# Kernel tuning notes

Hardware: AMD Instinct MI355X
Metric: run time of the kernel (lower is better)

## Reference

```python
import jax, jax.numpy as jnp
import numpy as np

NUM_HEADS = 4
NUM_POINTS = 8


def deform_attn_3d(q, value, ref, Hf, Wf, Wv, bv, Wo, bo, Wa, ba):
    # q: (BS,N,C)  value: (BS,Hf*Wf,C)  ref: (BS,N,D,2) normalized (x,y) in [0,1]
    BS, N, C = q.shape
    H, P = NUM_HEADS, NUM_POINTS
    D = ref.shape[2]
    c = C // H
    # value projection, split heads: (BS,H,M,c)
    v = (value @ Wv + bv).reshape(BS, Hf * Wf, H, c).transpose(0, 2, 1, 3)
    # sampling offsets and attention weights from the query
    off = (q @ Wo + bo).reshape(BS, N, H, P, 2)
    attn = jax.nn.softmax((q @ Wa + ba).reshape(BS, N, H, P), axis=-1)
    # normalize offsets by (W,H); distribute P points over D z-anchors (P//D per anchor)
    norm = jnp.array([Wf, Hf], dtype=q.dtype)
    off = off.reshape(BS, N, H, P // D, D, 2) / norm
    loc = (ref[:, :, None, None, :, :] + off).reshape(BS, N, H, P, 2)
    # grid_sample(align_corners=False, padding=zeros): pixel = loc*size - 0.5
    x = loc[..., 0] * Wf - 0.5
    y = loc[..., 1] * Hf - 0.5
    x0f = jnp.floor(x)
    y0f = jnp.floor(y)
    lx = x - x0f
    ly = y - y0f
    x0 = x0f.astype(jnp.int32)
    y0 = y0f.astype(jnp.int32)

    def tohead(a):  # (BS,N,H,P) -> (BS,H,N*P)
        return a.transpose(0, 2, 1, 3).reshape(BS, H, N * P)

    def gather(yy, xx):
        valid = ((xx >= 0) & (xx < Wf) & (yy >= 0) & (yy < Hf)).astype(q.dtype)
        idx = jnp.clip(yy, 0, Hf - 1) * Wf + jnp.clip(xx, 0, Wf - 1)
        g = jnp.take_along_axis(v, tohead(idx)[..., None], axis=2)  # (BS,H,N*P,c)
        return g * tohead(valid)[..., None]

    out = (gather(y0, x0) * tohead((1 - lx) * (1 - ly))[..., None]
           + gather(y0, x0 + 1) * tohead(lx * (1 - ly))[..., None]
           + gather(y0 + 1, x0) * tohead((1 - lx) * ly)[..., None]
           + gather(y0 + 1, x0 + 1) * tohead(lx * ly)[..., None])
    out = (out * tohead(attn)[..., None]).reshape(BS, H, N, P, c).sum(3)  # (BS,H,N,c)
    return out.transpose(0, 2, 1, 3).reshape(BS, N, C)


def spatial_cross_attention(query, query_pos, value, reference_points_cam, bev_mask,
                            Hf, Wf, Wv, bv, Wo, bo, Wa, ba, Wout, bout):
    # query/query_pos: (B,N,C); value: (S,M,B,C); ref: (S,B,N,D,2); bev_mask: (S,B,N,D)
    B, N, C = query.shape
    S, M = value.shape[0], value.shape[1]
    D = reference_points_cam.shape[3]
    q = query + query_pos
    # broadcast queries over cameras (mask-equivalent of the torch rebatch/compaction):
    # deformable attention is per-query independent, so computing all queries per cam
    # and masking invalid ones is the same math as rebatch+scatter.
    q_all = jnp.broadcast_to(q[:, None], (B, S, N, C)).reshape(B * S, N, C)
    v_all = value.transpose(2, 0, 1, 3).reshape(B * S, M, C)
    ref = reference_points_cam.transpose(1, 0, 2, 3, 4).reshape(B * S, N, D, 2)
    out = deform_attn_3d(q_all, v_all, ref, Hf, Wf, Wv, bv, Wo, bo, Wa, ba)
    out = out.reshape(B, S, N, C)
    mask_q = (bev_mask.sum(-1) > 0).astype(query.dtype)  # (S,B,N): query hits this cam
    slots = (out * mask_q.transpose(1, 0, 2)[..., None]).sum(1)  # (B,N,C)
    count = jnp.maximum(mask_q.sum(0), 1.0)  # (B,N) clamp(min=1)
    slots = slots / count[..., None]
    # output_proj, dropout (eval -> identity), residual with original query
    return slots @ Wout + bout + query


def setup_inputs() -> dict:
    B, S, N, Z, C = 1, 6, 16384, 8, 128
    Hf, Wf = 28, 50
    H, P = NUM_HEADS, NUM_POINTS
    rng = jax.random.key(0)
    ks = jax.random.split(rng, 12)
    return {
        "query": jax.random.normal(ks[0], (B, N, C), jnp.float32),
        "query_pos": 0.1 * jax.random.normal(ks[1], (B, N, C), jnp.float32),
        "value": jax.random.normal(ks[2], (S, Hf * Wf, B, C), jnp.float32),
        "reference_points_cam": jax.random.uniform(ks[3], (S, B, N, Z, 2), jnp.float32),
        "bev_mask": jax.random.randint(ks[4], (S, B, N, Z), 0, 2).astype(bool),
        "Wv": 0.02 * jax.random.normal(ks[5], (C, C), jnp.float32),
        "bv": jnp.zeros((C,), jnp.float32),
        "Wo": 0.02 * jax.random.normal(ks[6], (C, H * P * 2), jnp.float32),
        "bo": 0.5 * jax.random.normal(ks[7], (H * P * 2,), jnp.float32),
        "Wa": 0.02 * jax.random.normal(ks[8], (C, H * P), jnp.float32),
        "ba": jnp.zeros((H * P,), jnp.float32),
        "Wout": 0.02 * jax.random.normal(ks[9], (C, C), jnp.float32),
        "bout": jnp.zeros((C,), jnp.float32),
        "Hf": Hf,
        "Wf": Wf,
    }


def reference(query, query_pos, value, reference_points_cam, bev_mask,
              Wv, bv, Wo, bo, Wa, ba, Wout, bout, Hf, Wf):
    return spatial_cross_attention(query, query_pos, value, reference_points_cam, bev_mask,
                                   Hf, Wf, Wv, bv, Wo, bo, Wa, ba, Wout, bout)
```

## Files before the change

### kernel.cpp

```cpp
#include <hip/hip_runtime.h>

#define N_Q   16384
#define C_DIM 128
#define S_CAM 6
#define M_VAL 1400
#define D_Z   8
#define HF    28
#define WF    50
#define QPB   8

typedef float f32x2 __attribute__((ext_vector_type(2)));

__device__ __forceinline__ bool mask_any(const unsigned char* __restrict__ mask,
                                         int mflag, size_t mbase){
  if(mflag==0){
    int any=0;
    #pragma unroll
    for(int d=0;d<D_Z;d++) any |= mask[mbase+d];
    return any!=0;
  } else if(mflag==1){
    const int* mp = (const int*)mask;  int any=0;
    #pragma unroll
    for(int d=0;d<D_Z;d++) any |= mp[mbase+d];
    return any!=0;
  } else {
    const long long* mp = (const long long*)mask;  long long any=0;
    #pragma unroll
    for(int d=0;d<D_Z;d++) any |= mp[mbase+d];
    return any!=0;
  }
}

__device__ __forceinline__ void corner_acc(const uint4 cv, const float wgt,
                                           f32x2* __restrict__ acc2){
  const f32x2 w2 = {wgt, wgt};
  const unsigned dw[4] = {cv.x, cv.y, cv.z, cv.w};
  #pragma unroll
  for(int j=0;j<4;j++){
    acc2[j*2+0] += w2 * __builtin_amdgcn_cvt_pk_f32_fp8(dw[j], false);
    acc2[j*2+1] += w2 * __builtin_amdgcn_cvt_pk_f32_fp8(dw[j], true);
  }
}

__global__ __launch_bounds__(256)
void value_proj_kernel(const float* __restrict__ value,
                       const float* __restrict__ Wv,
                       const float* __restrict__ bv,
                       unsigned char* __restrict__ v8,
                       const unsigned char* __restrict__ mask,
                       int* __restrict__ flag){
  __shared__ float tile[8][C_DIM];
  __shared__ float part[8][C_DIM];
  __shared__ int s_cntA, s_cntB;
  const int tid = threadIdx.x;
  const int c   = tid & 127;
  const int kh  = tid >> 7;
  const int r0  = blockIdx.x * 8;
  if(blockIdx.x==0 && tid==0){ s_cntA=0; s_cntB=0; }
  {
    const float4* src = (const float4*)(value + (size_t)r0*C_DIM);
    ((float4*)&tile[0][0])[tid] = src[tid];
  }
  __syncthreads();
  float acc[8];
  {
    const float bias = kh ? 0.f : bv[c];
    #pragma unroll
    for(int r=0;r<8;r++) acc[r]=bias;
  }
  {
    const float* Wp = Wv + (size_t)kh*64*C_DIM + c;
    const int k00 = kh*64;
    for(int k0=0;k0<64;k0+=4){
      const float w0 = Wp[0];
      const float w1 = Wp[C_DIM];
      const float w2 = Wp[2*C_DIM];
      const float w3 = Wp[3*C_DIM];
      #pragma unroll
      for(int r=0;r<8;r++){
        const float4 t = *(const float4*)&tile[r][k00+k0];
        acc[r] += t.x*w0 + t.y*w1 + t.z*w2 + t.w*w3;
      }
      Wp += 4*C_DIM;
    }
  }
  if(kh){
    #pragma unroll
    for(int r=0;r<8;r++) part[r][c] = acc[r];
  }
  __syncthreads();
  if(!kh){
    #pragma unroll
    for(int r=0;r<8;r++){
      const float v = acc[r] + part[r][c];
      const int pk = __builtin_amdgcn_cvt_pk_fp8_f32(v, v, 0, false);
      v8[(size_t)(r0+r)*C_DIM + c] = (unsigned char)(pk & 0xff);
    }
  }
  if(blockIdx.x==0){
    int a=0, b=0;
    for(int i=tid;i<1024;i+=256){
      const unsigned char v = mask[i];
      if(((i&3)!=0) && v) a=1;
      if(((i&7)==4) && v) b=1;
    }
    if(a) atomicOr(&s_cntA,1);
    if(b) atomicOr(&s_cntB,1);
    __syncthreads();
    if(tid==0) flag[0] = s_cntA ? 0 : (s_cntB ? 1 : 2);
  }
}

__global__ __launch_bounds__(256)
void fused_deform_kernel(const unsigned char* __restrict__ v8,
                         const float* __restrict__ query,
                         const float* __restrict__ query_pos,
                         const float* __restrict__ Wo, const float* __restrict__ bo,
                         const float* __restrict__ Wa, const float* __restrict__ ba,
                         const float* __restrict__ ref,
                         const unsigned char* __restrict__ mask,
                         const int* __restrict__ flag,
                         const float* __restrict__ Wout,
                         const float* __restrict__ bout,
                         float* __restrict__ out){
  __shared__ float  qs[QPB][C_DIM+4];
  __shared__ float  offs[QPB][68];
  __shared__ float  attns[QPB][36];
  __shared__ float  logits[QPB][36];
  __shared__ float2 refs[QPB][S_CAM*D_Z+1];
  __shared__ int    activ[QPB][S_CAM];
  __shared__ float  cinv[QPB];

  const int tid = threadIdx.x;
  const int n0  = blockIdx.x * QPB;
  const int mflag = flag[0];
  const int qi = tid >> 5;
  const int l  = tid & 31;
  const int wi = tid >> 6;
  const int ln = tid & 63;
  const int kh = ln >> 5;
  const int cg = ln & 31;

  float2 rpre0, rpre1;
  {
    const int q0 = tid/48, r0 = tid%48;
    rpre0 = ((const float2*)ref)[((size_t)(r0>>3)*N_Q + (n0+q0))*D_Z + (r0&7)];
    if(tid < 128){
      const int e1 = tid + 256;
      const int q1 = e1/48, r1 = e1%48;
      rpre1 = ((const float2*)ref)[((size_t)(r1>>3)*N_Q + (n0+q1))*D_Z + (r1&7)];
    }
  }

  {
    const float4* qa = (const float4*)(query     + (size_t)n0*C_DIM);
    const float4* qb = (const float4*)(query_pos + (size_t)n0*C_DIM);
    const int r = tid >> 5, c4 = tid & 31;
    const float4 A = qa[tid], B = qb[tid];
    *(float4*)&qs[r][c4*4] = make_float4(A.x+B.x, A.y+B.y, A.z+B.z, A.w+B.w);
  }
  __syncthreads();

  {
    const int qA = 2*wi, qB = qA+1;
    float a0=0.f,a1=0.f,a2=0.f,a3=0.f, b0=0.f,b1=0.f,b2=0.f,b3=0.f;
    if(cg < 24){
      const float* Wp; int stride;
      if(cg < 16){ Wp = Wo + cg*4;      stride = 64; }
      else       { Wp = Wa + (cg-16)*4; stride = 32; }
      if(kh==0){
        const float4 bia = (cg<16) ? *(const float4*)&bo[cg*4]
                                   : *(const float4*)&ba[(cg-16)*4];
        a0=bia.x; a1=bia.y; a2=bia.z; a3=bia.w;
        b0=bia.x; b1=bia.y; b2=bia.z; b3=bia.w;
      }
      Wp += (size_t)kh*64*stride;
      const int k00 = kh*64;
      for(int k0=0;k0<64;k0+=4){
        const float4 qa = *(const float4*)&qs[qA][k00+k0];
        const float4 qb = *(const float4*)&qs[qB][k00+k0];
        const float4 w0 = *(const float4*)&Wp[0];
        const float4 w1 = *(const float4*)&Wp[stride];
        const float4 w2 = *(const float4*)&Wp[2*stride];
        const float4 w3 = *(const float4*)&Wp[3*stride];
        a0 += qa.x*w0.x + qa.y*w1.x + qa.z*w2.x + qa.w*w3.x;
        a1 += qa.x*w0.y + qa.y*w1.y + qa.z*w2.y + qa.w*w3.y;
        a2 += qa.x*w0.z + qa.y*w1.z + qa.z*w2.z + qa.w*w3.z;
        a3 += qa.x*w0.w + qa.y*w1.w + qa.z*w2.w + qa.w*w3.w;
        b0 += qb.x*w0.x + qb.y*w1.x + qb.z*w2.x + qb.w*w3.x;
        b1 += qb.x*w0.y + qb.y*w1.y + qb.z*w2.y + qb.w*w3.y;
        b2 += qb.x*w0.z + qb.y*w1.z + qb.z*w2.z + qb.w*w3.z;
        b3 += qb.x*w0.w + qb.y*w1.w + qb.z*w2.w + qb.w*w3.w;
        Wp += 4*stride;
      }
    }
    a0 += __shfl_xor(a0,32); a1 += __shfl_xor(a1,32);
    a2 += __shfl_xor(a2,32); a3 += __shfl_xor(a3,32);
    b0 += __shfl_xor(b0,32); b1 += __shfl_xor(b1,32);
    b2 += __shfl_xor(b2,32); b3 += __shfl_xor(b3,32);
    if(cg < 24){
      const float4 r = kh ? make_float4(b0,b1,b2,b3) : make_float4(a0,a1,a2,a3);
      const int q = qA + kh;
      if(cg < 16) *(float4*)&offs[q][cg*4] = r;
      else        *(float4*)&logits[q][(cg-16)*4] = r;
    }
  }
  {
    refs[tid/48][tid%48] = rpre0;
    if(tid < 128){
      const int e1 = tid + 256;
      refs[e1/48][e1%48] = rpre1;
    }
  }
  if(tid < QPB*S_CAM){
    const int q2 = tid / S_CAM, s = tid % S_CAM;
    activ[q2][s] = mask_any(mask, mflag, ((size_t)s*N_Q + (n0+q2))*D_Z) ? 1 : 0;
  }
  __syncthreads();
  if(tid < QPB*4){
    const int q2 = tid >> 2, h = tid & 3;
    const float* L = &logits[q2][h*8];
    float mx = L[0];
    #pragma unroll
    for(int p=1;p<8;p++) mx = fmaxf(mx, L[p]);
    float e[8], ssum = 0.f;
    #pragma unroll
    for(int p=0;p<8;p++){ e[p] = __expf(L[p]-mx); ssum += e[p]; }
    const float inv = 1.f/ssum;
    #pragma unroll
    for(int p=0;p<8;p++) attns[q2][h*8+p] = e[p]*inv;
  } else if(tid >= 256-QPB){
    const int q2 = tid - (256-QPB);
    int c = 0;
    #pragma unroll
    for(int s=0;s<S_CAM;s++) c += activ[q2][s];
    cinv[q2] = 1.f / fmaxf((float)c, 1.f);
  }
  __syncthreads();

  const int pg  = l >> 4;
  const int sg  = (l >> 3) & 1;
  const int ll  = l & 7;
  const int gch = ll*16;
  const int gh  = ll >> 1;
  f32x2 acc2[8];
  #pragma unroll
  for(int i=0;i<8;i++) acc2[i] = (f32x2){0.f, 0.f};

  for(int s=sg*3; s<sg*3+3; s++){
    if(!activ[qi][s]) continue;
    const unsigned char* vb = v8 + (size_t)s*M_VAL*C_DIM + gch;
    #pragma unroll 2
    for(int pp=0;pp<4;pp++){
      const int p = pg*4 + pp;
      const float2 r2 = refs[qi][s*8+p];
      const float ox = offs[qi][gh*16+p*2+0];
      const float oy = offs[qi][gh*16+p*2+1];
      const float x = fmaf(r2.x, (float)WF, ox - 0.5f);
      const float y = fmaf(r2.y, (float)HF, oy - 0.5f);
      const float x0f = floorf(x), y0f = floorf(y);
      const float fx = x - x0f,    fy = y - y0f;
      const int x0 = (int)x0f, y0 = (int)y0f;
      const int x1 = x0+1,     y1 = y0+1;
      const float at = attns[qi][gh*8+p];
      const float wx0 = (x0>=0 && x0<WF) ? (1.f-fx) : 0.f;
      const float wx1 = (x1>=0 && x1<WF) ? fx       : 0.f;
      const float wy0 = ((y0>=0 && y0<HF) ? (1.f-fy) : 0.f) * at;
      const float wy1 = ((y1>=0 && y1<HF) ? fy       : 0.f) * at;
      const int x0c = min(max(x0,0), WF-1), x1c = min(max(x1,0), WF-1);
      const int y0c = min(max(y0,0), HF-1), y1c = min(max(y1,0), HF-1);
      const float w00 = wx0*wy0, w01 = wx1*wy0, w10 = wx0*wy1, w11 = wx1*wy1;
      const uint4 c00 = *(const uint4*)(vb + (size_t)(y0c*WF+x0c)*C_DIM);
      const uint4 c01 = *(const uint4*)(vb + (size_t)(y0c*WF+x1c)*C_DIM);
      const uint4 c10 = *(const uint4*)(vb + (size_t)(y1c*WF+x0c)*C_DIM);
      const uint4 c11 = *(const uint4*)(vb + (size_t)(y1c*WF+x1c)*C_DIM);
      corner_acc(c00, w00, acc2);
      corner_acc(c01, w01, acc2);
      corner_acc(c10, w10, acc2);
      corner_acc(c11, w11, acc2);
    }
  }

  float* accf = (float*)acc2;
  #pragma unroll
  for(int i=0;i<16;i++) accf[i] += __shfl_xor(accf[i], 16);
  #pragma unroll
  for(int i=0;i<16;i++) accf[i] += __shfl_xor(accf[i], 8);
  if(l < 8){
    const float inv = cinv[qi];
    #pragma unroll
    for(int i=0;i<4;i++)
      *(float4*)&qs[qi][gch+i*4] = make_float4(accf[i*4+0]*inv, accf[i*4+1]*inv,
                                               accf[i*4+2]*inv, accf[i*4+3]*inv);
  }

  {
    const int qA = 2*wi, qB = qA+1;
    const int c0 = cg*4;
    float o0=0.f,o1=0.f,o2=0.f,o3=0.f, p0=0.f,p1=0.f,p2=0.f,p3=0.f;
    if(kh==0){
      const float4 bb = *(const float4*)&bout[c0];
      const float4 rA = *(const float4*)&query[(size_t)(n0+qA)*C_DIM + c0];
      const float4 rB = *(const float4*)&query[(size_t)(n0+qB)*C_DIM + c0];
      o0=bb.x+rA.x; o1=bb.y+rA.y; o2=bb.z+rA.z; o3=bb.w+rA.w;
      p0=bb.x+rB.x; p1=bb.y+rB.y; p2=bb.z+rB.z; p3=bb.w+rB.w;
    }
    const float* Wp = Wout + (size_t)kh*64*C_DIM + c0;
    const int k00 = kh*64;
    for(int k0=0;k0<64;k0+=4){
      const float4 sa = *(const float4*)&qs[qA][k00+k0];
      const float4 sb = *(const float4*)&qs[qB][k00+k0];
      const float4 w0 = *(const float4*)&Wp[0];
      const float4 w1 = *(const float4*)&Wp[C_DIM];
      const float4 w2 = *(const float4*)&Wp[2*C_DIM];
      const float4 w3 = *(const float4*)&Wp[3*C_DIM];
      o0 += sa.x*w0.x + sa.y*w1.x + sa.z*w2.x + sa.w*w3.x;
      o1 += sa.x*w0.y + sa.y*w1.y + sa.z*w2.y + sa.w*w3.y;
      o2 += sa.x*w0.z + sa.y*w1.z + sa.z*w2.z + sa.w*w3.z;
      o3 += sa.x*w0.w + sa.y*w1.w + sa.z*w2.w + sa.w*w3.w;
      p0 += sb.x*w0.x + sb.y*w1.x + sb.z*w2.x + sb.w*w3.x;
      p1 += sb.x*w0.y + sb.y*w1.y + sb.z*w2.y + sb.w*w3.y;
      p2 += sb.x*w0.z + sb.y*w1.z + sb.z*w2.z + sb.w*w3.z;
      p3 += sb.x*w0.w + sb.y*w1.w + sb.z*w2.w + sb.w*w3.w;
      Wp += 4*C_DIM;
    }
    o0 += __shfl_xor(o0,32); o1 += __shfl_xor(o1,32);
    o2 += __shfl_xor(o2,32); o3 += __shfl_xor(o3,32);
    p0 += __shfl_xor(p0,32); p1 += __shfl_xor(p1,32);
    p2 += __shfl_xor(p2,32); p3 += __shfl_xor(p3,32);
    const int n = n0 + qA + kh;
    const float4 r = kh ? make_float4(p0,p1,p2,p3) : make_float4(o0,o1,o2,o3);
    *(float4*)&out[(size_t)n*C_DIM + c0] = r;
  }
}

extern "C" void kernel_launch(void* const* d_in, const int* in_sizes, int n_in,
                              void* d_out, int out_size, void* d_ws, size_t ws_size,
                              hipStream_t stream){
  const float* query     = (const float*)d_in[0];
  const float* query_pos = (const float*)d_in[1];
  const float* value     = (const float*)d_in[2];
  const float* ref       = (const float*)d_in[3];
  const unsigned char* mask = (const unsigned char*)d_in[4];
  const float* Wv   = (const float*)d_in[5];
  const float* bv   = (const float*)d_in[6];
  const float* Wo   = (const float*)d_in[7];
  const float* bo   = (const float*)d_in[8];
  const float* Wa   = (const float*)d_in[9];
  const float* ba   = (const float*)d_in[10];
  const float* Wout = (const float*)d_in[11];
  const float* bout = (const float*)d_in[12];
  float* out = (float*)d_out;

  int* flag = (int*)d_ws;
  unsigned char* v8 = (unsigned char*)((char*)d_ws + 64);

  value_proj_kernel<<<(S_CAM*M_VAL)/8, 256, 0, stream>>>(value, Wv, bv, v8, mask, flag);
  fused_deform_kernel<<<N_Q/QPB, 256, 0, stream>>>(v8, query, query_pos,
                                                   Wo, bo, Wa, ba, ref, mask, flag,
                                                   Wout, bout, out);
}
```

Before: 166.0 us.

## Split fused deform kernel into prep, gather, and output-projection kernels

```diff
diff --git a/kernel.cpp b/kernel.cpp
--- a/kernel.cpp
+++ b/kernel.cpp
@@ -8,6 +8,8 @@
 #define HF    28
 #define WF    50
 #define QPB   8
+#define VP_BLOCKS 1050
+#define QP_BLOCKS 1024
 
 typedef float f32x2 __attribute__((ext_vector_type(2)));
 
@@ -42,91 +44,185 @@
   }
 }
 
+__device__ __forceinline__ void fma4(float4& a, const float4 t,
+                                     const float4 w0, const float4 w1,
+                                     const float4 w2, const float4 w3){
+  a.x += t.x*w0.x + t.y*w1.x + t.z*w2.x + t.w*w3.x;
+  a.y += t.x*w0.y + t.y*w1.y + t.z*w2.y + t.w*w3.y;
+  a.z += t.x*w0.z + t.y*w1.z + t.z*w2.z + t.w*w3.z;
+  a.w += t.x*w0.w + t.y*w1.w + t.z*w2.w + t.w*w3.w;
+}
+
+__device__ __forceinline__ void shfl4_add32(float4& a){
+  a.x += __shfl_xor(a.x, 32);
+  a.y += __shfl_xor(a.y, 32);
+  a.z += __shfl_xor(a.z, 32);
+  a.w += __shfl_xor(a.w, 32);
+}
+
 __global__ __launch_bounds__(256)
-void value_proj_kernel(const float* __restrict__ value,
-                       const float* __restrict__ Wv,
-                       const float* __restrict__ bv,
-                       unsigned char* __restrict__ v8,
-                       const unsigned char* __restrict__ mask,
-                       int* __restrict__ flag){
-  __shared__ float tile[8][C_DIM];
-  __shared__ float part[8][C_DIM];
+void prep_kernel(const float* __restrict__ value,
+                 const float* __restrict__ Wv,
+                 const float* __restrict__ bv,
+                 unsigned char* __restrict__ v8,
+                 const unsigned char* __restrict__ mask,
+                 int* __restrict__ flag,
+                 const float* __restrict__ query,
+                 const float* __restrict__ query_pos,
+                 const float* __restrict__ Wo, const float* __restrict__ bo,
+                 const float* __restrict__ Wa, const float* __restrict__ ba,
+                 float* __restrict__ out){
+  __shared__ float smem[2048];
+  __shared__ float lbuf[16][32];
   __shared__ int s_cntA, s_cntB;
   const int tid = threadIdx.x;
-  const int c   = tid & 127;
-  const int kh  = tid >> 7;
-  const int r0  = blockIdx.x * 8;
-  if(blockIdx.x==0 && tid==0){ s_cntA=0; s_cntB=0; }
-  {
-    const float4* src = (const float4*)(value + (size_t)r0*C_DIM);
-    ((float4*)&tile[0][0])[tid] = src[tid];
-  }
-  __syncthreads();
-  float acc[8];
-  {
-    const float bias = kh ? 0.f : bv[c];
-    #pragma unroll
-    for(int r=0;r<8;r++) acc[r]=bias;
-  }
-  {
-    const float* Wp = Wv + (size_t)kh*64*C_DIM + c;
-    const int k00 = kh*64;
-    for(int k0=0;k0<64;k0+=4){
-      const float w0 = Wp[0];
-      const float w1 = Wp[C_DIM];
-      const float w2 = Wp[2*C_DIM];
-      const float w3 = Wp[3*C_DIM];
+  const int bid = blockIdx.x;
+
+  if(bid < VP_BLOCKS){
+    float* tile = smem;
+    float* part = smem + 1024;
+    const int c   = tid & 127;
+    const int kh  = tid >> 7;
+    const int r0  = bid * 8;
+    if(bid==0 && tid==0){ s_cntA=0; s_cntB=0; }
+    {
+      const float4* src = (const float4*)(value + (size_t)r0*C_DIM);
+      ((float4*)tile)[tid] = src[tid];
+    }
+    __syncthreads();
+    float acc[8];
+    {
+      const float bias = kh ? 0.f : bv[c];
+      #pragma unroll
+      for(int r=0;r<8;r++) acc[r]=bias;
+    }
+    {
+      const float* Wp = Wv + (size_t)kh*64*C_DIM + c;
+      const int k00 = kh*64;
+      for(int k0=0;k0<64;k0+=4){
+        const float w0 = Wp[0];
+        const float w1 = Wp[C_DIM];
+        const float w2 = Wp[2*C_DIM];
+        const float w3 = Wp[3*C_DIM];
+        #pragma unroll
+        for(int r=0;r<8;r++){
+          const float4 t = *(const float4*)&tile[r*C_DIM + k00+k0];
+          acc[r] += t.x*w0 + t.y*w1 + t.z*w2 + t.w*w3;
+        }
+        Wp += 4*C_DIM;
+      }
+    }
+    if(kh){
+      #pragma unroll
+      for(int r=0;r<8;r++) part[r*C_DIM + c] = acc[r];
+    }
+    __syncthreads();
+    if(!kh){
       #pragma unroll
       for(int r=0;r<8;r++){
-        const float4 t = *(const float4*)&tile[r][k00+k0];
-        acc[r] += t.x*w0 + t.y*w1 + t.z*w2 + t.w*w3;
-      }
-      Wp += 4*C_DIM;
-    }
-  }
-  if(kh){
-    #pragma unroll
-    for(int r=0;r<8;r++) part[r][c] = acc[r];
-  }
-  __syncthreads();
-  if(!kh){
-    #pragma unroll
-    for(int r=0;r<8;r++){
-      const float v = acc[r] + part[r][c];
-      const int pk = __builtin_amdgcn_cvt_pk_fp8_f32(v, v, 0, false);
-      v8[(size_t)(r0+r)*C_DIM + c] = (unsigned char)(pk & 0xff);
-    }
-  }
-  if(blockIdx.x==0){
-    int a=0, b=0;
-    for(int i=tid;i<1024;i+=256){
-      const unsigned char v = mask[i];
-      if(((i&3)!=0) && v) a=1;
-      if(((i&7)==4) && v) b=1;
-    }
-    if(a) atomicOr(&s_cntA,1);
-    if(b) atomicOr(&s_cntB,1);
+        const float v = acc[r] + part[r*C_DIM + c];
+        const int pk = __builtin_amdgcn_cvt_pk_fp8_f32(v, v, 0, false);
+        v8[(size_t)(r0+r)*C_DIM + c] = (unsigned char)(pk & 0xff);
+      }
+    }
+    if(bid==0){
+      int a=0, b=0;
+      for(int i=tid;i<1024;i+=256){
+        const unsigned char v = mask[i];
+        if(((i&3)!=0) && v) a=1;
+        if(((i&7)==4) && v) b=1;
+      }
+      if(a) atomicOr(&s_cntA,1);
+      if(b) atomicOr(&s_cntB,1);
+      __syncthreads();
+      if(tid==0) flag[0] = s_cntA ? 0 : (s_cntB ? 1 : 2);
+    }
+  } else {
+    const int qb = bid - VP_BLOCKS;
+    const int n0 = qb * 16;
+    float* qtile = smem;
+    {
+      const float4* qa = (const float4*)(query     + (size_t)n0*C_DIM);
+      const float4* qp = (const float4*)(query_pos + (size_t)n0*C_DIM);
+      #pragma unroll
+      for(int j=0;j<2;j++){
+        const int idx = tid + 256*j;
+        const float4 A = qa[idx], B = qp[idx];
+        *(float4*)&qtile[idx*4] = make_float4(A.x+B.x, A.y+B.y, A.z+B.z, A.w+B.w);
+      }
+    }
     __syncthreads();
-    if(tid==0) flag[0] = s_cntA ? 0 : (s_cntB ? 1 : 2);
+    const int wi = tid >> 6;
+    const int ln = tid & 63;
+    const int kh = ln >> 5;
+    const int cg = ln & 31;
+    float4 a0={0,0,0,0}, a1={0,0,0,0}, a2={0,0,0,0}, a3={0,0,0,0};
+    if(cg < 24){
+      const float* Wp; int stride; const float* bptr;
+      if(cg < 16){ Wp = Wo + cg*4;      stride = 64; bptr = &bo[cg*4]; }
+      else       { Wp = Wa + (cg-16)*4; stride = 32; bptr = &ba[(cg-16)*4]; }
+      if(kh==0){
+        const float4 bb = *(const float4*)bptr;
+        a0=bb; a1=bb; a2=bb; a3=bb;
+      }
+      Wp += (size_t)kh*64*stride;
+      const float* q0 = &qtile[(wi*4+0)*C_DIM + kh*64];
+      const float* q1 = &qtile[(wi*4+1)*C_DIM + kh*64];
+      const float* q2 = &qtile[(wi*4+2)*C_DIM + kh*64];
+      const float* q3 = &qtile[(wi*4+3)*C_DIM + kh*64];
+      #pragma unroll 4
+      for(int k0=0;k0<64;k0+=4){
+        const float4 w0 = *(const float4*)&Wp[0];
+        const float4 w1 = *(const float4*)&Wp[stride];
+        const float4 w2 = *(const float4*)&Wp[2*stride];
+        const float4 w3 = *(const float4*)&Wp[3*stride];
+        fma4(a0, *(const float4*)&q0[k0], w0,w1,w2,w3);
+        fma4(a1, *(const float4*)&q1[k0], w0,w1,w2,w3);
+        fma4(a2, *(const float4*)&q2[k0], w0,w1,w2,w3);
+        fma4(a3, *(const float4*)&q3[k0], w0,w1,w2,w3);
+        Wp += 4*stride;
+      }
+    }
+    shfl4_add32(a0); shfl4_add32(a1); shfl4_add32(a2); shfl4_add32(a3);
+    if(cg < 16){
+      const int c0 = cg*4;
+      const int r  = wi*4 + kh*2;
+      const float4 sA = kh ? a2 : a0;
+      const float4 sB = kh ? a3 : a1;
+      *(float4*)&out[(size_t)(n0+r  )*C_DIM + c0] = sA;
+      *(float4*)&out[(size_t)(n0+r+1)*C_DIM + c0] = sB;
+    } else if(cg < 24){
+      const int c0 = (cg-16)*4;
+      const int r  = wi*4 + kh*2;
+      *(float4*)&lbuf[r  ][c0] = kh ? a2 : a0;
+      *(float4*)&lbuf[r+1][c0] = kh ? a3 : a1;
+    }
+    __syncthreads();
+    if(tid < 64){
+      const int q = tid >> 2, h = tid & 3;
+      const float* L = &lbuf[q][h*8];
+      float mx = L[0];
+      #pragma unroll
+      for(int p=1;p<8;p++) mx = fmaxf(mx, L[p]);
+      float e[8], ssum = 0.f;
+      #pragma unroll
+      for(int p=0;p<8;p++){ e[p] = __expf(L[p]-mx); ssum += e[p]; }
+      const float inv = 1.f/ssum;
+      float* dst = &out[(size_t)(n0+q)*C_DIM + 64 + h*8];
+      *(float4*)dst     = make_float4(e[0]*inv, e[1]*inv, e[2]*inv, e[3]*inv);
+      *(float4*)(dst+4) = make_float4(e[4]*inv, e[5]*inv, e[6]*inv, e[7]*inv);
+    }
   }
 }
 
 __global__ __launch_bounds__(256)
-void fused_deform_kernel(const unsigned char* __restrict__ v8,
-                         const float* __restrict__ query,
-                         const float* __restrict__ query_pos,
-                         const float* __restrict__ Wo, const float* __restrict__ bo,
-                         const float* __restrict__ Wa, const float* __restrict__ ba,
-                         const float* __restrict__ ref,
-                         const unsigned char* __restrict__ mask,
-                         const int* __restrict__ flag,
-                         const float* __restrict__ Wout,
-                         const float* __restrict__ bout,
-                         float* __restrict__ out){
-  __shared__ float  qs[QPB][C_DIM+4];
+void gather_kernel(const unsigned char* __restrict__ v8,
+                   const float* __restrict__ ref,
+                   const unsigned char* __restrict__ mask,
+                   const int* __restrict__ flag,
+                   float* __restrict__ out){
   __shared__ float  offs[QPB][68];
   __shared__ float  attns[QPB][36];
-  __shared__ float  logits[QPB][36];
   __shared__ float2 refs[QPB][S_CAM*D_Z+1];
   __shared__ int    activ[QPB][S_CAM];
   __shared__ float  cinv[QPB];
@@ -136,104 +232,31 @@
   const int mflag = flag[0];
   const int qi = tid >> 5;
   const int l  = tid & 31;
-  const int wi = tid >> 6;
-  const int ln = tid & 63;
-  const int kh = ln >> 5;
-  const int cg = ln & 31;
-
-  float2 rpre0, rpre1;
+
+  if(tid < 192){
+    const int q = tid/24, j = tid%24;
+    const float4 v = *(const float4*)&out[(size_t)(n0+q)*C_DIM + j*4];
+    if(j<16) *(float4*)&offs[q][j*4] = v;
+    else     *(float4*)&attns[q][(j-16)*4] = v;
+  }
   {
-    const int q0 = tid/48, r0 = tid%48;
-    rpre0 = ((const float2*)ref)[((size_t)(r0>>3)*N_Q + (n0+q0))*D_Z + (r0&7)];
+    const int q = tid/48, r = tid%48;
+    refs[q][r] = ((const float2*)ref)[((size_t)(r>>3)*N_Q + (n0+q))*D_Z + (r&7)];
     if(tid < 128){
       const int e1 = tid + 256;
       const int q1 = e1/48, r1 = e1%48;
-      rpre1 = ((const float2*)ref)[((size_t)(r1>>3)*N_Q + (n0+q1))*D_Z + (r1&7)];
-    }
-  }
-
-  {
-    const float4* qa = (const float4*)(query     + (size_t)n0*C_DIM);
-    const float4* qb = (const float4*)(query_pos + (size_t)n0*C_DIM);
-    const int r = tid >> 5, c4 = tid & 31;
-    const float4 A = qa[tid], B = qb[tid];
-    *(float4*)&qs[r][c4*4] = make_float4(A.x+B.x, A.y+B.y, A.z+B.z, A.w+B.w);
-  }
-  __syncthreads();
-
-  {
-    const int qA = 2*wi, qB = qA+1;
-    float a0=0.f,a1=0.f,a2=0.f,a3=0.f, b0=0.f,b1=0.f,b2=0.f,b3=0.f;
-    if(cg < 24){
-      const float* Wp; int stride;
-      if(cg < 16){ Wp = Wo + cg*4;      stride = 64; }
-      else       { Wp = Wa + (cg-16)*4; stride = 32; }
-      if(kh==0){
-        const float4 bia = (cg<16) ? *(const float4*)&bo[cg*4]
-                                   : *(const float4*)&ba[(cg-16)*4];
-        a0=bia.x; a1=bia.y; a2=bia.z; a3=bia.w;
-        b0=bia.x; b1=bia.y; b2=bia.z; b3=bia.w;
-      }
-      Wp += (size_t)kh*64*stride;
-      const int k00 = kh*64;
-      for(int k0=0;k0<64;k0+=4){
-        const float4 qa = *(const float4*)&qs[qA][k00+k0];
-        const float4 qb = *(const float4*)&qs[qB][k00+k0];
-        const float4 w0 = *(const float4*)&Wp[0];
-        const float4 w1 = *(const float4*)&Wp[stride];
-        const float4 w2 = *(const float4*)&Wp[2*stride];
-        const float4 w3 = *(const float4*)&Wp[3*stride];
-        a0 += qa.x*w0.x + qa.y*w1.x + qa.z*w2.x + qa.w*w3.x;
-        a1 += qa.x*w0.y + qa.y*w1.y + qa.z*w2.y + qa.w*w3.y;
-        a2 += qa.x*w0.z + qa.y*w1.z + qa.z*w2.z + qa.w*w3.z;
-        a3 += qa.x*w0.w + qa.y*w1.w + qa.z*w2.w + qa.w*w3.w;
-        b0 += qb.x*w0.x + qb.y*w1.x + qb.z*w2.x + qb.w*w3.x;
-        b1 += qb.x*w0.y + qb.y*w1.y + qb.z*w2.y + qb.w*w3.y;
-        b2 += qb.x*w0.z + qb.y*w1.z + qb.z*w2.z + qb.w*w3.z;
-        b3 += qb.x*w0.w + qb.y*w1.w + qb.z*w2.w + qb.w*w3.w;
-        Wp += 4*stride;
-      }
-    }
-    a0 += __shfl_xor(a0,32); a1 += __shfl_xor(a1,32);
-    a2 += __shfl_xor(a2,32); a3 += __shfl_xor(a3,32);
-    b0 += __shfl_xor(b0,32); b1 += __shfl_xor(b1,32);
-    b2 += __shfl_xor(b2,32); b3 += __shfl_xor(b3,32);
-    if(cg < 24){
-      const float4 r = kh ? make_float4(b0,b1,b2,b3) : make_float4(a0,a1,a2,a3);
-      const int q = qA + kh;
-      if(cg < 16) *(float4*)&offs[q][cg*4] = r;
-      else        *(float4*)&logits[q][(cg-16)*4] = r;
-    }
-  }
-  {
-    refs[tid/48][tid%48] = rpre0;
-    if(tid < 128){
-      const int e1 = tid + 256;
-      refs[e1/48][e1%48] = rpre1;
+      refs[q1][r1] = ((const float2*)ref)[((size_t)(r1>>3)*N_Q + (n0+q1))*D_Z + (r1&7)];
     }
   }
   if(tid < QPB*S_CAM){
     const int q2 = tid / S_CAM, s = tid % S_CAM;
     activ[q2][s] = mask_any(mask, mflag, ((size_t)s*N_Q + (n0+q2))*D_Z) ? 1 : 0;
-  }
-  __syncthreads();
-  if(tid < QPB*4){
-    const int q2 = tid >> 2, h = tid & 3;
-    const float* L = &logits[q2][h*8];
-    float mx = L[0];
-    #pragma unroll
-    for(int p=1;p<8;p++) mx = fmaxf(mx, L[p]);
-    float e[8], ssum = 0.f;
-    #pragma unroll
-    for(int p=0;p<8;p++){ e[p] = __expf(L[p]-mx); ssum += e[p]; }
-    const float inv = 1.f/ssum;
-    #pragma unroll
-    for(int p=0;p<8;p++) attns[q2][h*8+p] = e[p]*inv;
-  } else if(tid >= 256-QPB){
-    const int q2 = tid - (256-QPB);
+  } else if(tid < QPB*S_CAM + QPB){
+    const int q2 = tid - QPB*S_CAM;
     int c = 0;
     #pragma unroll
-    for(int s=0;s<S_CAM;s++) c += activ[q2][s];
+    for(int s=0;s<S_CAM;s++)
+      c += mask_any(mask, mflag, ((size_t)s*N_Q + (n0+q2))*D_Z) ? 1 : 0;
     cinv[q2] = 1.f / fmaxf((float)c, 1.f);
   }
   __syncthreads();
@@ -288,49 +311,75 @@
   for(int i=0;i<16;i++) accf[i] += __shfl_xor(accf[i], 8);
   if(l < 8){
     const float inv = cinv[qi];
+    float* dst = &out[(size_t)(n0+qi)*C_DIM + gch];
     #pragma unroll
     for(int i=0;i<4;i++)
-      *(float4*)&qs[qi][gch+i*4] = make_float4(accf[i*4+0]*inv, accf[i*4+1]*inv,
-                                               accf[i*4+2]*inv, accf[i*4+3]*inv);
-  }
+      *(float4*)&dst[i*4] = make_float4(accf[i*4+0]*inv, accf[i*4+1]*inv,
+                                        accf[i*4+2]*inv, accf[i*4+3]*inv);
+  }
+}
+
+__global__ __launch_bounds__(256)
+void outproj_kernel(const float* __restrict__ Wout,
+                    const float* __restrict__ bout,
+                    const float* __restrict__ query,
+                    float* __restrict__ out){
+  __shared__ float stile[4][4][C_DIM];
+  const int tid = threadIdx.x;
+  const int n0  = blockIdx.x * 16;
+  const int wi  = tid >> 6;
+  const int ln  = tid & 63;
+  const int kh  = ln >> 5;
+  const int cg  = ln & 31;
 
   {
-    const int qA = 2*wi, qB = qA+1;
-    const int c0 = cg*4;
-    float o0=0.f,o1=0.f,o2=0.f,o3=0.f, p0=0.f,p1=0.f,p2=0.f,p3=0.f;
-    if(kh==0){
-      const float4 bb = *(const float4*)&bout[c0];
-      const float4 rA = *(const float4*)&query[(size_t)(n0+qA)*C_DIM + c0];
-      const float4 rB = *(const float4*)&query[(size_t)(n0+qB)*C_DIM + c0];
-      o0=bb.x+rA.x; o1=bb.y+rA.y; o2=bb.z+rA.z; o3=bb.w+rA.w;
-      p0=bb.x+rB.x; p1=bb.y+rB.y; p2=bb.z+rB.z; p3=bb.w+rB.w;
-    }
-    const float* Wp = Wout + (size_t)kh*64*C_DIM + c0;
-    const int k00 = kh*64;
+    const float4* src = (const float4*)(out + (size_t)(n0 + wi*4)*C_DIM);
+    #pragma unroll
+    for(int j=0;j<2;j++){
+      const int idx = ln + 64*j;
+      const int r = idx >> 5, c4 = idx & 31;
+      *(float4*)&stile[wi][r][c4*4] = src[idx];
+    }
+  }
+  float4 a0={0,0,0,0}, a1={0,0,0,0}, a2={0,0,0,0}, a3={0,0,0,0};
+  {
+    const float* Wp = Wout + (size_t)kh*64*C_DIM + cg*4;
+    const float* s0 = &stile[wi][0][kh*64];
+    const float* s1 = &stile[wi][1][kh*64];
+    const float* s2 = &stile[wi][2][kh*64];
+    const float* s3 = &stile[wi][3][kh*64];
+    #pragma unroll 4
     for(int k0=0;k0<64;k0+=4){
-      const float4 sa = *(const float4*)&qs[qA][k00+k0];
-      const float4 sb = *(const float4*)&qs[qB][k00+k0];
       const float4 w0 = *(const float4*)&Wp[0];
       const float4 w1 = *(const float4*)&Wp[C_DIM];
       const float4 w2 = *(const float4*)&Wp[2*C_DIM];
       const float4 w3 = *(const float4*)&Wp[3*C_DIM];
-      o0 += sa.x*w0.x + sa.y*w1.x + sa.z*w2.x + sa.w*w3.x;
-      o1 += sa.x*w0.y + sa.y*w1.y + sa.z*w2.y + sa.w*w3.y;
-      o2 += sa.x*w0.z + sa.y*w1.z + sa.z*w2.z + sa.w*w3.z;
-      o3 += sa.x*w0.w + sa.y*w1.w + sa.z*w2.w + sa.w*w3.w;
-      p0 += sb.x*w0.x + sb.y*w1.x + sb.z*w2.x + sb.w*w3.x;
-      p1 += sb.x*w0.y + sb.y*w1.y + sb.z*w2.y + sb.w*w3.y;
-      p2 += sb.x*w0.z + sb.y*w1.z + sb.z*w2.z + sb.w*w3.z;
-      p3 += sb.x*w0.w + sb.y*w1.w + sb.z*w2.w + sb.w*w3.w;
+      fma4(a0, *(const float4*)&s0[k0], w0,w1,w2,w3);
+      fma4(a1, *(const float4*)&s1[k0], w0,w1,w2,w3);
+      fma4(a2, *(const float4*)&s2[k0], w0,w1,w2,w3);
+      fma4(a3, *(const float4*)&s3[k0], w0,w1,w2,w3);
       Wp += 4*C_DIM;
     }
-    o0 += __shfl_xor(o0,32); o1 += __shfl_xor(o1,32);
-    o2 += __shfl_xor(o2,32); o3 += __shfl_xor(o3,32);
-    p0 += __shfl_xor(p0,32); p1 += __shfl_xor(p1,32);
-    p2 += __shfl_xor(p2,32); p3 += __shfl_xor(p3,32);
-    const int n = n0 + qA + kh;
-    const float4 r = kh ? make_float4(p0,p1,p2,p3) : make_float4(o0,o1,o2,o3);
-    *(float4*)&out[(size_t)n*C_DIM + c0] = r;
+  }
+  shfl4_add32(a0); shfl4_add32(a1); shfl4_add32(a2); shfl4_add32(a3);
+  {
+    const int c0 = cg*4;
+    const float4 bb = *(const float4*)&bout[c0];
+    const int r = wi*4 + kh*2;
+    const float4 sA = kh ? a2 : a0;
+    const float4 sB = kh ? a3 : a1;
+    {
+      const int n = n0 + r;
+      const float4 rq = *(const float4*)&query[(size_t)n*C_DIM + c0];
+      *(float4*)&out[(size_t)n*C_DIM + c0] =
+        make_float4(sA.x+bb.x+rq.x, sA.y+bb.y+rq.y, sA.z+bb.z+rq.z, sA.w+bb.w+rq.w);
+    }
+    {
+      const int n = n0 + r + 1;
+      const float4 rq = *(const float4*)&query[(size_t)n*C_DIM + c0];
+      *(float4*)&out[(size_t)n*C_DIM + c0] =
+        make_float4(sB.x+bb.x+rq.x, sB.y+bb.y+rq.y, sB.z+bb.z+rq.z, sB.w+bb.w+rq.w);
+    }
   }
 }
 
@@ -355,8 +404,8 @@
   int* flag = (int*)d_ws;
   unsigned char* v8 = (unsigned char*)((char*)d_ws + 64);
 
-  value_proj_kernel<<<(S_CAM*M_VAL)/8, 256, 0, stream>>>(value, Wv, bv, v8, mask, flag);
-  fused_deform_kernel<<<N_Q/QPB, 256, 0, stream>>>(v8, query, query_pos,
-                                                   Wo, bo, Wa, ba, ref, mask, flag,
-                                                   Wout, bout, out);
-}
+  prep_kernel<<<VP_BLOCKS + QP_BLOCKS, 256, 0, stream>>>(
+      value, Wv, bv, v8, mask, flag, query, query_pos, Wo, bo, Wa, ba, out);
+  gather_kernel<<<N_Q/QPB, 256, 0, stream>>>(v8, ref, mask, flag, out);
+  outproj_kernel<<<N_Q/16, 256, 0, stream>>>(Wout, bout, query, out);
+}
```

After: 175.3 us. 5.6% more time.
